# Kernel optimization log

Measured on AMD Instinct MI355X. Metric: run time of the kernel, lower is better.

The kernel has to match this reference:

```python
import jax, jax.numpy as jnp
import numpy as np

SMILE_LEN = 40


def _gru_cell(x, h, Wih, Whh, bih, bhh):
    # PyTorch GRU gate order: r, z, n
    gi = x @ Wih.T + bih          # [B, 3H]
    gh = h @ Whh.T + bhh          # [B, 3H]
    H = h.shape[-1]
    ir, iz, inn = gi[:, :H], gi[:, H:2 * H], gi[:, 2 * H:]
    hr, hz, hn = gh[:, :H], gh[:, H:2 * H], gh[:, 2 * H:]
    r = jax.nn.sigmoid(ir + hr)
    z = jax.nn.sigmoid(iz + hz)
    n = jnp.tanh(inn + r * hn)
    return (1.0 - z) * n + z * h


def setup_inputs() -> dict:
    key = jax.random.key(0)
    ks = jax.random.split(key, 12)
    B, L, H, A = 16384, 128, 256, 21
    s = 0.05
    return {
        "latent": jax.random.normal(ks[0], (B, L), jnp.float32),
        "W1": jax.random.normal(ks[1], (H, L), jnp.float32) * s,
        "b1": jax.random.normal(ks[2], (H,), jnp.float32) * s,
        "W2": jax.random.normal(ks[3], (H, H), jnp.float32) * s,
        "b2": jax.random.normal(ks[4], (H,), jnp.float32) * s,
        "Wih": jax.random.normal(ks[5], (3 * H, A), jnp.float32) * s,
        "Whh": jax.random.normal(ks[6], (3 * H, H), jnp.float32) * s,
        "bih": jax.random.normal(ks[7], (3 * H,), jnp.float32) * s,
        "bhh": jax.random.normal(ks[8], (3 * H,), jnp.float32) * s,
        "Wd": jax.random.normal(ks[9], (A, H), jnp.float32) * s,
        "bd": jax.random.normal(ks[10], (A,), jnp.float32) * s,
    }


def reference(latent, W1, b1, W2, b2, Wih, Whh, bih, bhh, Wd, bd):
    B = latent.shape[0]
    A = Wih.shape[1]
    # latent -> Dense -> ReLU -> (Dropout: identity in eval) -> Dense
    hidden = jax.nn.relu(latent @ W1.T + b1) @ W2.T + b2  # [B, H]
    # start token: +32 at position 0, -32 elsewhere
    start = jnp.full((B, A), -32.0, jnp.float32).at[:, 0].set(32.0)

    def step(carry, _):
        h, inp = carry
        h_new = _gru_cell(inp, h, Wih, Whh, bih, bhh)
        pred = h_new @ Wd.T + bd                      # [B, A]
        return (h_new, jax.lax.stop_gradient(pred)), pred

    (_, _), preds = jax.lax.scan(step, (hidden, start), None, length=SMILE_LEN - 1)
    # preds: [T-1, B, A] -> y: [B, T, A] with start token at t=0
    y = jnp.concatenate([start[:, None, :], jnp.transpose(preds, (1, 0, 2))], axis=1)
    return y
```

## Files before the change

kernel.cpp:

```cpp
#include <hip/hip_runtime.h>
#include <hip/hip_bf16.h>


typedef __bf16 bf16x8 __attribute__((ext_vector_type(8)));
typedef float  f32x16 __attribute__((ext_vector_type(16)));

#define MFMA32(a,b,c) __builtin_amdgcn_mfma_f32_32x32x16_bf16((a),(b),(c),0,0,0)
#define WAITV(n) asm volatile("s_waitcnt vmcnt(" #n ")" ::: "memory")
#define LGKM0()  asm volatile("s_waitcnt lgkmcnt(0)" ::: "memory")
#define BARRIER() do { asm volatile("" ::: "memory"); __builtin_amdgcn_s_barrier(); asm volatile("" ::: "memory"); } while (0)

static constexpr int A_DIM = 21;

static constexpr size_t O_W1F   = 0;
static constexpr size_t O_W2F   = O_W1F + 256*128*2;
static constexpr size_t O_ST1   = O_W2F + 256*256*2;
static constexpr size_t O_WMN   = O_ST1 + 8*16*3*1024;
static constexpr size_t O_BMAIN = O_WMN + 8*16*5*1024;
static constexpr size_t O_GI1   = O_BMAIN + 1024*4;


__global__ void prep_frag(const float* __restrict__ src, __bf16* __restrict__ dst,
                          int SR, int SC, int NF, int NCH) {
  int total = NF * NCH * 512;
  for (int i = blockIdx.x * blockDim.x + threadIdx.x; i < total;
       i += gridDim.x * blockDim.x) {
    int fragid = i >> 9, within = i & 511;
    int lane = within >> 3, j = within & 7;
    int nf = fragid / NCH, kc = fragid - nf * NCH;
    int n = nf * 32 + (lane & 31);
    int k = kc * 16 + (lane >> 5) * 8 + j;
    float v = (n < SR && k < SC) ? src[n * SC + k] : 0.f;
    dst[i] = (__bf16)v;
  }
}

__global__ void prep_st1(const float* __restrict__ Whh, __bf16* __restrict__ dst) {
  int total = 8 * 16 * 3 * 512;
  for (int i = blockIdx.x * blockDim.x + threadIdx.x; i < total;
       i += gridDim.x * blockDim.x) {
    int j = i & 7, lane = (i >> 3) & 63;
    int slice = i >> 9;
    int g = slice % 3, kc = (slice / 3) & 15, w = slice / 48;
    int n = g * 256 + w * 32 + (lane & 31);
    int k = kc * 16 + (lane >> 5) * 8 + j;
    dst[i] = (__bf16)Whh[n * 256 + k];
  }
}

__global__ void prep_main(const float* __restrict__ Whh, const float* __restrict__ Wih,
                          const float* __restrict__ Wd, __bf16* __restrict__ dst) {
  int total = 8 * 16 * 5 * 512;
  for (int i = blockIdx.x * blockDim.x + threadIdx.x; i < total;
       i += gridDim.x * blockDim.x) {
    int j = i & 7, lane = (i >> 3) & 63;
    int slice = i >> 9;
    int g = slice % 5, kc = (slice / 5) & 15, w = slice / 80;
    int k = kc * 16 + (lane >> 5) * 8 + j;
    float v = 0.f;
    if (g == 4) {
      int n = lane & 31;
      v = (n < A_DIM) ? Wd[n * 256 + k] : 0.f;
    } else {
      int n = g * 256 + w * 32 + (lane & 31);
      if (n < 768) v = Whh[n * 256 + k];
      if (n < 512 || n >= 768) {
        int nn = (n < 512) ? n : (n - 256);
        float d = 0.f;
        #pragma unroll
        for (int q = 0; q < A_DIM; ++q) d += Wih[nn * A_DIM + q] * Wd[q * 256 + k];
        v += d;
      }
    }
    dst[i] = (__bf16)v;
  }
}

__global__ void prep_bias(const float* __restrict__ Wih, const float* __restrict__ bih,
                          const float* __restrict__ bhh, const float* __restrict__ bd,
                          float* __restrict__ bmain, float* __restrict__ gi1c) {
  int i = blockIdx.x * blockDim.x + threadIdx.x;
  if (i < 1024) {
    float bm;
    if (i < 512) {
      float d = 0.f;
      #pragma unroll
      for (int q = 0; q < A_DIM; ++q) d += Wih[i * A_DIM + q] * bd[q];
      bm = bhh[i] + bih[i] + d;
    } else if (i < 768) {
      bm = bhh[i];
    } else {
      int nn = i - 256;
      float d = 0.f;
      #pragma unroll
      for (int q = 0; q < A_DIM; ++q) d += Wih[nn * A_DIM + q] * bd[q];
      bm = bih[nn] + d;
    }
    bmain[i] = bm;
  }
  if (i < 768) {
    float s = 32.f * Wih[i * A_DIM + 0];
    #pragma unroll
    for (int q = 1; q < A_DIM; ++q) s -= 32.f * Wih[i * A_DIM + q];
    gi1c[i] = s + bih[i];
  }
}


__device__ __forceinline__ void gload16(const void* g, void* l) {
  __builtin_amdgcn_global_load_lds((const __attribute__((address_space(1))) void*)g,
                                   (__attribute__((address_space(3))) void*)l, 16, 0, 0);
}

__device__ __forceinline__ bf16x8 lds_frag(const __bf16* base, int rowBytes,
                                           int row, int kb) {
  return *(const bf16x8*)((const char*)base + row * rowBytes +
                          (kb ^ ((row & 7) << 4)));
}

__device__ __forceinline__ void gru_gate(const f32x16& ar, const f32x16& az,
                                         const f32x16& ah, const f32x16& ai,
                                         f32x16& hr) {
  #pragma unroll
  for (int g = 0; g < 16; ++g) {
    float r = __builtin_amdgcn_rcpf(1.f + __builtin_amdgcn_exp2f(ar[g] * -1.442695041f));
    float z = __builtin_amdgcn_rcpf(1.f + __builtin_amdgcn_exp2f(az[g] * -1.442695041f));
    float pre = ai[g] + r * ah[g];
    float e = __builtin_amdgcn_exp2f(pre * 2.885390082f);
    float n = 1.f - 2.f * __builtin_amdgcn_rcpf(e + 1.f);
    hr[g] = n + z * (hr[g] - n);
  }
}

__device__ __forceinline__ void write_h(__bf16* hl, int c, int hfv,
                                        const f32x16& hr0, const f32x16& hr1) {
  #pragma unroll
  for (int g = 0; g < 16; ++g) {
    int pat = (g & 3) + 8 * (g >> 2) + 4 * hfv;
    int sw = (2 * c) ^ ((pat & 7) << 4);
    *(__bf16*)((char*)hl + pat * 512 + sw)        = (__bf16)hr0[g];
    *(__bf16*)((char*)hl + (32 + pat) * 512 + sw) = (__bf16)hr1[g];
  }
}

__global__ __launch_bounds__(512, 2) void decoder_main(
    const float* __restrict__ latent, const float* __restrict__ b1,
    const float* __restrict__ b2, const float* __restrict__ bhh,
    const float* __restrict__ bd, const float* __restrict__ gi1c,
    const float* __restrict__ bmain,
    const __bf16* __restrict__ W1f, const __bf16* __restrict__ W2f,
    const __bf16* __restrict__ St1, const __bf16* __restrict__ Wmn,
    float* __restrict__ y) {
  __shared__ __attribute__((aligned(16))) __bf16 h_lds[64 * 256];
  __shared__ __attribute__((aligned(16))) char ringmem[8 * 3 * 5120];

  const int tid = threadIdx.x;
  const int w = tid >> 6;
  const int l = tid & 63;
  const int lc = l & 31;
  const int hfv = l >> 5;
  const int b0 = blockIdx.x * 64;
  const int c = w * 32 + lc;

  __bf16* lat_al = (__bf16*)(ringmem);
  __bf16* h1_al  = (__bf16*)(ringmem + 16384);

  for (int i = tid; i < 64 * A_DIM; i += 512) {
    int r = i / A_DIM, a = i - r * A_DIM;
    y[(size_t)(b0 + r) * 840 + a] = (a == 0) ? 32.f : -32.f;
  }

  for (int i = tid; i < 64 * 32; i += 512) {
    int r = i >> 5, c4 = i & 31;
    const float4 v = *(const float4*)(latent + (size_t)(b0 + r) * 128 + c4 * 4);
    __bf16* q = (__bf16*)((char*)lat_al + r * 256 + ((c4 * 8) ^ ((r & 7) << 4)));
    q[0] = (__bf16)v.x; q[1] = (__bf16)v.y; q[2] = (__bf16)v.z; q[3] = (__bf16)v.w;
  }
  __syncthreads();

  const bf16x8* W1v = (const bf16x8*)W1f;
  const bf16x8* W2v = (const bf16x8*)W2f;

  f32x16 acc0, acc1;
  {
    const float bb = b1[c];
    #pragma unroll
    for (int i = 0; i < 16; ++i) { acc0[i] = bb; acc1[i] = bb; }
  }
  #pragma unroll
  for (int kc = 0; kc < 8; ++kc) {
    bf16x8 a0 = lds_frag(lat_al, 256, lc, kc * 32 + hfv * 16);
    bf16x8 a1 = lds_frag(lat_al, 256, 32 + lc, kc * 32 + hfv * 16);
    bf16x8 bw = W1v[(w * 8 + kc) * 64 + l];
    acc0 = MFMA32(a0, bw, acc0);
    acc1 = MFMA32(a1, bw, acc1);
  }
  #pragma unroll
  for (int g = 0; g < 16; ++g) {
    int pat = (g & 3) + 8 * (g >> 2) + 4 * hfv;
    int sw = (2 * c) ^ ((pat & 7) << 4);
    float v0 = acc0[g] > 0.f ? acc0[g] : 0.f;
    float v1 = acc1[g] > 0.f ? acc1[g] : 0.f;
    *(__bf16*)((char*)h1_al + pat * 512 + sw)        = (__bf16)v0;
    *(__bf16*)((char*)h1_al + (32 + pat) * 512 + sw) = (__bf16)v1;
  }
  __syncthreads();

  f32x16 hr0, hr1;
  {
    const float bb = b2[c];
    #pragma unroll
    for (int i = 0; i < 16; ++i) { hr0[i] = bb; hr1[i] = bb; }
  }
  #pragma unroll
  for (int kc = 0; kc < 16; ++kc) {
    bf16x8 a0 = lds_frag(h1_al, 512, lc, kc * 32 + hfv * 16);
    bf16x8 a1 = lds_frag(h1_al, 512, 32 + lc, kc * 32 + hfv * 16);
    bf16x8 bw = W2v[(w * 16 + kc) * 64 + l];
    hr0 = MFMA32(a0, bw, hr0);
    hr1 = MFMA32(a1, bw, hr1);
  }
  write_h(h_lds, c, hfv, hr0, hr1);
  __syncthreads();

  const float i_r1 = bhh[c] + gi1c[c];
  const float i_z1 = bhh[256 + c] + gi1c[256 + c];
  const float i_h1 = bhh[512 + c];
  const float i_n1 = gi1c[512 + c];
  const float i_rm = bmain[c];
  const float i_zm = bmain[256 + c];
  const float i_hm = bmain[512 + c];
  const float i_nm = bmain[768 + c];
  const float pb = (lc < A_DIM) ? bd[lc] : 0.f;

  char* ringw = ringmem + w * 15360;
  const char* sW1 = (const char*)St1 + w * 49152 + (size_t)l * 16;
  const char* sW  = (const char*)Wmn + w * 81920 + (size_t)l * 16;

  f32x16 aR0, aR1, aZ0, aZ1, aH0, aH1, aI0, aI1, pacc;

  #pragma unroll
  for (int p = 0; p < 2; ++p)
    #pragma unroll
    for (int g = 0; g < 3; ++g)
      gload16(sW1 + p * 3072 + g * 1024, ringw + p * 5120 + g * 1024);

  #pragma unroll
  for (int i = 0; i < 16; ++i) {
    aR0[i] = i_r1; aR1[i] = i_r1; aZ0[i] = i_z1; aZ1[i] = i_z1;
    aH0[i] = i_h1; aH1[i] = i_h1; aI0[i] = i_n1; aI1[i] = i_n1;
  }
  #pragma unroll
  for (int kc = 0; kc < 16; ++kc) {
    if (kc < 14) {
      const int fi = (kc + 2) % 3;
      #pragma unroll
      for (int g = 0; g < 3; ++g)
        gload16(sW1 + (kc + 2) * 3072 + g * 1024, ringw + fi * 5120 + g * 1024);
    }
    if (kc < 14) { WAITV(6); } else if (kc == 14) { WAITV(3); } else { WAITV(0); }
    const char* fc = ringw + (kc % 3) * 5120 + (size_t)l * 16;
    bf16x8 a0 = lds_frag(h_lds, 512, lc, kc * 32 + hfv * 16);
    bf16x8 a1 = lds_frag(h_lds, 512, 32 + lc, kc * 32 + hfv * 16);
    bf16x8 br = *(const bf16x8*)(fc);
    bf16x8 bz = *(const bf16x8*)(fc + 1024);
    bf16x8 bh = *(const bf16x8*)(fc + 2048);
    aR0 = MFMA32(a0, br, aR0); aR1 = MFMA32(a1, br, aR1);
    aZ0 = MFMA32(a0, bz, aZ0); aZ1 = MFMA32(a1, bz, aZ1);
    aH0 = MFMA32(a0, bh, aH0); aH1 = MFMA32(a1, bh, aH1);
  }

  #pragma unroll
  for (int p = 0; p < 2; ++p) {
    #pragma unroll
    for (int g = 0; g < 4; ++g)
      gload16(sW + p * 5120 + g * 1024, ringw + p * 5120 + g * 1024);
    if (w < 2) gload16(sW + p * 5120 + 4096, ringw + p * 5120 + 4096);
  }

  gru_gate(aR0, aZ0, aH0, aI0, hr0);
  gru_gate(aR1, aZ1, aH1, aI1, hr1);
  LGKM0(); BARRIER();
  write_h(h_lds, c, hfv, hr0, hr1);
  LGKM0(); BARRIER();

  int base = 0;
  #pragma unroll 1
  for (int t = 2; t <= 39; ++t) {
    #pragma unroll
    for (int i = 0; i < 16; ++i) {
      aR0[i] = i_rm; aR1[i] = i_rm; aZ0[i] = i_zm; aZ1[i] = i_zm;
      aH0[i] = i_hm; aH1[i] = i_hm; aI0[i] = i_nm; aI1[i] = i_nm;
      pacc[i] = pb;
    }
    #pragma unroll
    for (int kc = 0; kc < 16; ++kc) {
      {
        int f2 = (kc + 2) % 3 + base; if (f2 >= 3) f2 -= 3;
        const char* gsrc = sW + ((kc + 2) & 15) * 5120;
        char* fd = ringw + f2 * 5120;
        gload16(gsrc,        fd);
        gload16(gsrc + 1024, fd + 1024);
        gload16(gsrc + 2048, fd + 2048);
        gload16(gsrc + 3072, fd + 3072);
        if (w < 2) gload16(gsrc + 4096, fd + 4096);
      }
      WAITV(8);
      int f0i = kc % 3 + base; if (f0i >= 3) f0i -= 3;
      const char* fc = ringw + f0i * 5120 + (size_t)l * 16;
      bf16x8 a0 = lds_frag(h_lds, 512, lc, kc * 32 + hfv * 16);
      bf16x8 a1 = lds_frag(h_lds, 512, 32 + lc, kc * 32 + hfv * 16);
      bf16x8 br = *(const bf16x8*)(fc);
      bf16x8 bz = *(const bf16x8*)(fc + 1024);
      bf16x8 bh = *(const bf16x8*)(fc + 2048);
      bf16x8 bi = *(const bf16x8*)(fc + 3072);
      aR0 = MFMA32(a0, br, aR0); aR1 = MFMA32(a1, br, aR1);
      aZ0 = MFMA32(a0, bz, aZ0); aZ1 = MFMA32(a1, bz, aZ1);
      aH0 = MFMA32(a0, bh, aH0); aH1 = MFMA32(a1, bh, aH1);
      aI0 = MFMA32(a0, bi, aI0); aI1 = MFMA32(a1, bi, aI1);
      if (w < 2) {
        bf16x8 bp = *(const bf16x8*)(fc + 4096);
        pacc = MFMA32(w ? a1 : a0, bp, pacc);
      }
    }
    if (w < 2 && lc < A_DIM) {
      #pragma unroll
      for (int g = 0; g < 16; ++g) {
        int pat = (g & 3) + 8 * (g >> 2) + 4 * hfv;
        y[(size_t)(b0 + 32 * w + pat) * 840 + (size_t)(t - 1) * 21 + lc] = pacc[g];
      }
    }
    gru_gate(aR0, aZ0, aH0, aI0, hr0);
    gru_gate(aR1, aZ1, aH1, aI1, hr1);
    LGKM0(); BARRIER();
    write_h(h_lds, c, hfv, hr0, hr1);
    LGKM0(); BARRIER();
    base = (base == 2) ? 0 : base + 1;
  }

  if (w < 2) {
    #pragma unroll
    for (int i = 0; i < 16; ++i) pacc[i] = pb;
    #pragma unroll
    for (int kc = 0; kc < 16; ++kc) {
      bf16x8 a = lds_frag(h_lds, 512, 32 * w + lc, kc * 32 + hfv * 16);
      bf16x8 bp = *(const bf16x8*)((const char*)Wmn + (size_t)(kc * 5 + 4) * 1024 +
                                   (size_t)l * 16);
      pacc = MFMA32(a, bp, pacc);
    }
    if (lc < A_DIM) {
      #pragma unroll
      for (int g = 0; g < 16; ++g) {
        int pat = (g & 3) + 8 * (g >> 2) + 4 * hfv;
        y[(size_t)(b0 + 32 * w + pat) * 840 + 39 * 21 + lc] = pacc[g];
      }
    }
  }
  WAITV(0);
}

extern "C" void kernel_launch(void* const* d_in, const int* in_sizes, int n_in,
                              void* d_out, int out_size, void* d_ws, size_t ws_size,
                              hipStream_t stream) {
  const float* latent = (const float*)d_in[0];
  const float* W1 = (const float*)d_in[1];
  const float* b1 = (const float*)d_in[2];
  const float* W2 = (const float*)d_in[3];
  const float* b2 = (const float*)d_in[4];
  const float* Wih = (const float*)d_in[5];
  const float* Whh = (const float*)d_in[6];
  const float* bih = (const float*)d_in[7];
  const float* bhh = (const float*)d_in[8];
  const float* Wd = (const float*)d_in[9];
  const float* bd = (const float*)d_in[10];
  float* y = (float*)d_out;
  char* ws = (char*)d_ws;

  __bf16* W1f = (__bf16*)(ws + O_W1F);
  __bf16* W2f = (__bf16*)(ws + O_W2F);
  __bf16* St1 = (__bf16*)(ws + O_ST1);
  __bf16* Wmn = (__bf16*)(ws + O_WMN);
  float* bmain = (float*)(ws + O_BMAIN);
  float* gi1c = (float*)(ws + O_GI1);

  prep_frag<<<128, 256, 0, stream>>>(W1, W1f, 256, 128, 8, 8);
  prep_frag<<<256, 256, 0, stream>>>(W2, W2f, 256, 256, 8, 16);
  prep_st1<<<512, 256, 0, stream>>>(Whh, St1);
  prep_main<<<1024, 256, 0, stream>>>(Whh, Wih, Wd, Wmn);
  prep_bias<<<4, 256, 0, stream>>>(Wih, bih, bhh, bd, bmain, gi1c);

  decoder_main<<<256, 512, 0, stream>>>(latent, b1, b2, bhh, bd, gi1c, bmain,
                                        W1f, W2f, St1, Wmn, y);
}
```

Baseline: 1.450 ms.

## Keep Wd fragments resident in LDS and stagger per-block weight chunk order

The output projection weights move out of the per-step streamed weight ring into a dedicated LDS buffer that is loaded once per block. This shrinks each ring slot and removes an extra global-to-LDS load per chunk for two waves. Each block also rotates the order in which it walks the 16 K-chunks by a block-dependent phase, so concurrent blocks read different weight chunks and L2/channel hot-spotting is reduced. The cost is 16 KB more LDS use and slightly more index arithmetic.

Result: faster. 1.333 ms (-8.1%).

```diff
diff --git a/kernel.cpp b/kernel.cpp
--- a/kernel.cpp
+++ b/kernel.cpp
@@ -16,7 +16,8 @@
 static constexpr size_t O_W2F   = O_W1F + 256*128*2;
 static constexpr size_t O_ST1   = O_W2F + 256*256*2;
 static constexpr size_t O_WMN   = O_ST1 + 8*16*3*1024;
-static constexpr size_t O_BMAIN = O_WMN + 8*16*5*1024;
+static constexpr size_t O_WDF   = O_WMN + 8*16*4*1024;
+static constexpr size_t O_BMAIN = O_WDF + 16*1024;
 static constexpr size_t O_GI1   = O_BMAIN + 1024*4;
 
 
@@ -50,27 +51,22 @@
 
 __global__ void prep_main(const float* __restrict__ Whh, const float* __restrict__ Wih,
                           const float* __restrict__ Wd, __bf16* __restrict__ dst) {
-  int total = 8 * 16 * 5 * 512;
+  int total = 8 * 16 * 4 * 512;
   for (int i = blockIdx.x * blockDim.x + threadIdx.x; i < total;
        i += gridDim.x * blockDim.x) {
     int j = i & 7, lane = (i >> 3) & 63;
     int slice = i >> 9;
-    int g = slice % 5, kc = (slice / 5) & 15, w = slice / 80;
+    int g = slice & 3, kc = (slice >> 2) & 15, w = slice >> 6;
     int k = kc * 16 + (lane >> 5) * 8 + j;
+    int n = g * 256 + w * 32 + (lane & 31);
     float v = 0.f;
-    if (g == 4) {
-      int n = lane & 31;
-      v = (n < A_DIM) ? Wd[n * 256 + k] : 0.f;
-    } else {
-      int n = g * 256 + w * 32 + (lane & 31);
-      if (n < 768) v = Whh[n * 256 + k];
-      if (n < 512 || n >= 768) {
-        int nn = (n < 512) ? n : (n - 256);
-        float d = 0.f;
-        #pragma unroll
-        for (int q = 0; q < A_DIM; ++q) d += Wih[nn * A_DIM + q] * Wd[q * 256 + k];
-        v += d;
-      }
+    if (n < 768) v = Whh[n * 256 + k];
+    if (n < 512 || n >= 768) {
+      int nn = (n < 512) ? n : (n - 256);
+      float d = 0.f;
+      #pragma unroll
+      for (int q = 0; q < A_DIM; ++q) d += Wih[nn * A_DIM + q] * Wd[q * 256 + k];
+      v += d;
     }
     dst[i] = (__bf16)v;
   }
@@ -150,9 +146,10 @@
     const float* __restrict__ bmain,
     const __bf16* __restrict__ W1f, const __bf16* __restrict__ W2f,
     const __bf16* __restrict__ St1, const __bf16* __restrict__ Wmn,
-    float* __restrict__ y) {
+    const __bf16* __restrict__ Wdf, float* __restrict__ y) {
   __shared__ __attribute__((aligned(16))) __bf16 h_lds[64 * 256];
-  __shared__ __attribute__((aligned(16))) char ringmem[8 * 3 * 5120];
+  __shared__ __attribute__((aligned(16))) char wd_lds[16 * 1024];
+  __shared__ __attribute__((aligned(16))) char ringmem[8 * 3 * 4096];
 
   const int tid = threadIdx.x;
   const int w = tid >> 6;
@@ -161,6 +158,7 @@
   const int hfv = l >> 5;
   const int b0 = blockIdx.x * 64;
   const int c = w * 32 + lc;
+  const int ph = (blockIdx.x >> 3) & 15;
 
   __bf16* lat_al = (__bf16*)(ringmem);
   __bf16* h1_al  = (__bf16*)(ringmem + 16384);
@@ -233,9 +231,12 @@
   const float i_nm = bmain[768 + c];
   const float pb = (lc < A_DIM) ? bd[lc] : 0.f;
 
-  char* ringw = ringmem + w * 15360;
+  char* ringw = ringmem + w * 12288;
   const char* sW1 = (const char*)St1 + w * 49152 + (size_t)l * 16;
-  const char* sW  = (const char*)Wmn + w * 81920 + (size_t)l * 16;
+  const char* sW  = (const char*)Wmn + w * 65536 + (size_t)l * 16;
+
+  gload16((const char*)Wdf + (w * 2 + 0) * 1024 + (size_t)l * 16, wd_lds + (w * 2 + 0) * 1024);
+  gload16((const char*)Wdf + (w * 2 + 1) * 1024 + (size_t)l * 16, wd_lds + (w * 2 + 1) * 1024);
 
   f32x16 aR0, aR1, aZ0, aZ1, aH0, aH1, aI0, aI1, pacc;
 
@@ -243,7 +244,7 @@
   for (int p = 0; p < 2; ++p)
     #pragma unroll
     for (int g = 0; g < 3; ++g)
-      gload16(sW1 + p * 3072 + g * 1024, ringw + p * 5120 + g * 1024);
+      gload16(sW1 + ((p + ph) & 15) * 3072 + g * 1024, ringw + p * 4096 + g * 1024);
 
   #pragma unroll
   for (int i = 0; i < 16; ++i) {
@@ -252,16 +253,18 @@
   }
   #pragma unroll
   for (int kc = 0; kc < 16; ++kc) {
+    const int kcp = (kc + ph) & 15;
     if (kc < 14) {
       const int fi = (kc + 2) % 3;
+      const int kcp2 = (kc + 2 + ph) & 15;
       #pragma unroll
       for (int g = 0; g < 3; ++g)
-        gload16(sW1 + (kc + 2) * 3072 + g * 1024, ringw + fi * 5120 + g * 1024);
+        gload16(sW1 + kcp2 * 3072 + g * 1024, ringw + fi * 4096 + g * 1024);
     }
     if (kc < 14) { WAITV(6); } else if (kc == 14) { WAITV(3); } else { WAITV(0); }
-    const char* fc = ringw + (kc % 3) * 5120 + (size_t)l * 16;
-    bf16x8 a0 = lds_frag(h_lds, 512, lc, kc * 32 + hfv * 16);
-    bf16x8 a1 = lds_frag(h_lds, 512, 32 + lc, kc * 32 + hfv * 16);
+    const char* fc = ringw + (kc % 3) * 4096 + (size_t)l * 16;
+    bf16x8 a0 = lds_frag(h_lds, 512, lc, kcp * 32 + hfv * 16);
+    bf16x8 a1 = lds_frag(h_lds, 512, 32 + lc, kcp * 32 + hfv * 16);
     bf16x8 br = *(const bf16x8*)(fc);
     bf16x8 bz = *(const bf16x8*)(fc + 1024);
     bf16x8 bh = *(const bf16x8*)(fc + 2048);
@@ -272,10 +275,12 @@
 
   #pragma unroll
   for (int p = 0; p < 2; ++p) {
-    #pragma unroll
-    for (int g = 0; g < 4; ++g)
-      gload16(sW + p * 5120 + g * 1024, ringw + p * 5120 + g * 1024);
-    if (w < 2) gload16(sW + p * 5120 + 4096, ringw + p * 5120 + 4096);
+    const char* gsrc = sW + ((p + ph) & 15) * 4096;
+    char* fd = ringw + p * 4096;
+    gload16(gsrc,        fd);
+    gload16(gsrc + 1024, fd + 1024);
+    gload16(gsrc + 2048, fd + 2048);
+    gload16(gsrc + 3072, fd + 3072);
   }
 
   gru_gate(aR0, aZ0, aH0, aI0, hr0);
@@ -295,21 +300,21 @@
     }
     #pragma unroll
     for (int kc = 0; kc < 16; ++kc) {
+      const int kcp = (kc + ph) & 15;
       {
         int f2 = (kc + 2) % 3 + base; if (f2 >= 3) f2 -= 3;
-        const char* gsrc = sW + ((kc + 2) & 15) * 5120;
-        char* fd = ringw + f2 * 5120;
+        const char* gsrc = sW + ((kc + 2 + ph) & 15) * 4096;
+        char* fd = ringw + f2 * 4096;
         gload16(gsrc,        fd);
         gload16(gsrc + 1024, fd + 1024);
         gload16(gsrc + 2048, fd + 2048);
         gload16(gsrc + 3072, fd + 3072);
-        if (w < 2) gload16(gsrc + 4096, fd + 4096);
       }
       WAITV(8);
       int f0i = kc % 3 + base; if (f0i >= 3) f0i -= 3;
-      const char* fc = ringw + f0i * 5120 + (size_t)l * 16;
-      bf16x8 a0 = lds_frag(h_lds, 512, lc, kc * 32 + hfv * 16);
-      bf16x8 a1 = lds_frag(h_lds, 512, 32 + lc, kc * 32 + hfv * 16);
+      const char* fc = ringw + f0i * 4096 + (size_t)l * 16;
+      bf16x8 a0 = lds_frag(h_lds, 512, lc, kcp * 32 + hfv * 16);
+      bf16x8 a1 = lds_frag(h_lds, 512, 32 + lc, kcp * 32 + hfv * 16);
       bf16x8 br = *(const bf16x8*)(fc);
       bf16x8 bz = *(const bf16x8*)(fc + 1024);
       bf16x8 bh = *(const bf16x8*)(fc + 2048);
@@ -319,7 +324,7 @@
       aH0 = MFMA32(a0, bh, aH0); aH1 = MFMA32(a1, bh, aH1);
       aI0 = MFMA32(a0, bi, aI0); aI1 = MFMA32(a1, bi, aI1);
       if (w < 2) {
-        bf16x8 bp = *(const bf16x8*)(fc + 4096);
+        bf16x8 bp = *(const bf16x8*)(wd_lds + kcp * 1024 + (size_t)l * 16);
         pacc = MFMA32(w ? a1 : a0, bp, pacc);
       }
     }
@@ -344,8 +349,7 @@
     #pragma unroll
     for (int kc = 0; kc < 16; ++kc) {
       bf16x8 a = lds_frag(h_lds, 512, 32 * w + lc, kc * 32 + hfv * 16);
-      bf16x8 bp = *(const bf16x8*)((const char*)Wmn + (size_t)(kc * 5 + 4) * 1024 +
-                                   (size_t)l * 16);
+      bf16x8 bp = *(const bf16x8*)(wd_lds + kc * 1024 + (size_t)l * 16);
       pacc = MFMA32(a, bp, pacc);
     }
     if (lc < A_DIM) {
@@ -380,15 +384,17 @@
   __bf16* W2f = (__bf16*)(ws + O_W2F);
   __bf16* St1 = (__bf16*)(ws + O_ST1);
   __bf16* Wmn = (__bf16*)(ws + O_WMN);
+  __bf16* Wdf = (__bf16*)(ws + O_WDF);
   float* bmain = (float*)(ws + O_BMAIN);
   float* gi1c = (float*)(ws + O_GI1);
 
   prep_frag<<<128, 256, 0, stream>>>(W1, W1f, 256, 128, 8, 8);
   prep_frag<<<256, 256, 0, stream>>>(W2, W2f, 256, 256, 8, 16);
+  prep_frag<<<32, 256, 0, stream>>>(Wd, Wdf, 21, 256, 1, 16);
   prep_st1<<<512, 256, 0, stream>>>(Whh, St1);
   prep_main<<<1024, 256, 0, stream>>>(Whh, Wih, Wd, Wmn);
   prep_bias<<<4, 256, 0, stream>>>(Wih, bih, bhh, bd, bmain, gi1c);
 
   decoder_main<<<256, 512, 0, stream>>>(latent, b1, b2, bhh, bd, gi1c, bmain,
-                                        W1f, W2f, St1, Wmn, y);
-}
+                                        W1f, W2f, St1, Wmn, Wdf, y);
+}
```
